# Kernel tuning notes

Hardware: AMD Instinct MI355X
Metric: run time of the kernel (lower is better)

## Reference

```python
import jax, jax.numpy as jnp
import numpy as np
from jax import lax

DN = ('NCHW', 'OIHW', 'NCHW')

def _winit(key, fan_in, shape):
    return (jax.random.uniform(key, shape) - 0.5) * 2 * 2.4 / fan_in ** 0.5

def setup_inputs() -> dict:
    key = jax.random.key(0)
    ks = jax.random.split(key, 6)
    B = 131072
    x = jax.random.normal(ks[0], (B, 1, 16, 16), dtype=jnp.float32)
    H1w = _winit(ks[1], 5 * 5 * 1, (12, 1, 5, 5))
    H1b = jnp.zeros((12, 8, 8), jnp.float32)
    H2w = _winit(ks[2], 5 * 5 * 8, (12, 8, 5, 5))
    H2b = jnp.zeros((12, 4, 4), jnp.float32)
    H3w = _winit(ks[3], 4 * 4 * 12, (4 * 4 * 12, 30))
    H3b = jnp.zeros((30,), jnp.float32)
    outw = _winit(ks[4], 30, (30, 10))
    outb = jnp.zeros((10,), jnp.float32)
    return {"x": x, "H1w": H1w, "H1b": H1b, "H2w": H2w, "H2b": H2b,
            "H3w": H3w, "H3b": H3b, "outw": outw, "outb": outb}

def _pad_m1(x):
    # constant pad of 2 on H and W with value -1.0
    return jnp.pad(x, ((0, 0), (0, 0), (2, 2), (2, 2)), constant_values=-1.0)

def _conv_s2(x, w):
    return lax.conv_general_dilated(x, w, window_strides=(2, 2),
                                    padding='VALID', dimension_numbers=DN)

def reference(x, H1w, H1b, H2w, H2b, H3w, H3b, outw, outb):
    # eval mode: no roll augmentation, dropout is identity
    x = _pad_m1(x)                                   # [B,1,20,20]
    x = _conv_s2(x, H1w) + H1b                       # [B,12,8,8]
    x = jax.nn.relu(x)
    x = _pad_m1(x)                                   # [B,12,12,12]
    s1 = _conv_s2(x[:, 0:8], H2w[0:4])               # [B,4,4,4]
    s2 = _conv_s2(x[:, 4:12], H2w[4:8])              # [B,4,4,4]
    s3 = _conv_s2(jnp.concatenate((x[:, 0:4], x[:, 8:12]), axis=1), H2w[8:12])
    x = jnp.concatenate((s1, s2, s3), axis=1) + H2b  # [B,12,4,4]
    x = jax.nn.relu(x)
    x = x.reshape(x.shape[0], -1)                    # [B,192]
    x = jax.nn.relu(x @ H3w + H3b)                   # [B,30]
    return x @ outw + outb                           # [B,10]
```

## Files before the change

### kernel.cpp

```cpp
#include <hip/hip_runtime.h>
#include <hip/hip_fp16.h>

typedef _Float16 f16x8 __attribute__((ext_vector_type(8)));
typedef float f32x4 __attribute__((ext_vector_type(4)));

union U4H8 { uint4 u; f16x8 h; };
__device__ inline f16x8 asH(uint4 u){ U4H8 x; x.u = u; return x.h; }
__device__ inline unsigned int pk(float a, float b){
    __half2 h = __floats2half2_rn(a, b);
    union { __half2 h; unsigned int u; } c; c.h = h; return c.u;
}
__device__ inline unsigned int pkr(float a, float b){
    return pk(fmaxf(a, 0.f), fmaxf(b, 0.f));
}
__device__ inline unsigned short h16(float a){
    union { __half h; unsigned short s; } c; c.h = __float2half(a); return c.s;
}

#define NFRAG 28
#define WS_B1 7168
#define WS_B2 8192
#define WS_B3 8448
#define WS_B4 8960

__global__ __launch_bounds__(256) void build_tables(
    const float* __restrict__ H1w, const float* __restrict__ H1b,
    const float* __restrict__ H2w, const float* __restrict__ H2b,
    const float* __restrict__ H3w, const float* __restrict__ H3b,
    const float* __restrict__ outw, const float* __restrict__ outb,
    unsigned int* __restrict__ ws)
{
    const int t = threadIdx.x, b = blockIdx.x;
    float* wsf = (float*)ws;

    if (b < NFRAG) {
        if (t < 64) {
            const int lane = t, ch = lane >> 4, oc = lane & 15;
            const int fi = b;
            unsigned short us[8];
            for (int j = 0; j < 8; ++j) {
                float w = 0.f;
                if (fi < 2) {
                    int kh = fi * 4 + ch;
                    if (kh < 5 && j < 5 && oc < 12) w = H1w[oc * 25 + kh * 5 + j];
                } else if (fi < 15) {
                    int kk = fi - 2;
                    int tap = kk * 2 + (ch >> 1);
                    int ic = (ch & 1) * 8 + j;
                    if (tap < 25 && oc < 12) {
                        int kh = tap / 5, kw = tap % 5;
                        int q = oc >> 2, icl = -1;
                        if (q == 0)      { if (ic < 8) icl = ic; }
                        else if (q == 1) { if (ic >= 4 && ic < 12) icl = ic - 4; }
                        else             { if (ic < 4) icl = ic;
                                           else if (ic >= 8 && ic < 12) icl = ic - 4; }
                        if (icl >= 0) w = H2w[((oc * 8 + icl) * 5 + kh) * 5 + kw];
                    }
                } else if (fi < 27) {
                    int idx = fi - 15, nt = idx / 6, kk = idx % 6;
                    int k = kk * 32 + ch * 8 + j;
                    int pos = k / 12, oc2 = k % 12;
                    int col = nt * 16 + oc;
                    if (col < 30) w = H3w[(oc2 * 16 + pos) * 30 + col];
                } else {
                    int k = ch * 8 + j;
                    if (k < 30 && oc < 10) w = outw[k * 10 + oc];
                }
                us[j] = h16(w);
            }
            uint4 u;
            u.x = us[0] | ((unsigned int)us[1] << 16);
            u.y = us[2] | ((unsigned int)us[3] << 16);
            u.z = us[4] | ((unsigned int)us[5] << 16);
            u.w = us[6] | ((unsigned int)us[7] << 16);
            ((uint4*)ws)[fi * 64 + lane] = u;
        }
    } else if (b == NFRAG) {
        for (int idx = t; idx < 1024; idx += 256) {
            int e = idx >> 6, l2 = idx & 63;
            int tt = e >> 2, r = e & 3;
            int oc = 4 * (l2 >> 4) + r, m2 = l2 & 15;
            int oh = 2 * tt + (m2 >> 3), ow = m2 & 7;
            float v = 0.f;
            if (oc < 12) {
                v = H1b[oc * 64 + oh * 8 + ow];
                for (int kh = 0; kh < 5; ++kh)
                    for (int kw = 0; kw < 5; ++kw) {
                        int rr = 2 * oh + kh, cc = 2 * ow + kw;
                        if (rr < 2 || rr >= 18 || cc < 2 || cc >= 18)
                            v -= H1w[oc * 25 + kh * 5 + kw];
                    }
            }
            wsf[WS_B1 + e * 64 + l2] = v;
        }
    } else {
        {
            int e = t >> 6, l2 = t & 63;
            int oc = 4 * (l2 >> 4) + e, m2 = l2 & 15;
            int oh = m2 >> 2, ow = m2 & 3;
            float v = 0.f;
            if (oc < 12) {
                v = H2b[oc * 16 + oh * 4 + ow];
                for (int icl = 0; icl < 8; ++icl)
                    for (int kh = 0; kh < 5; ++kh)
                        for (int kw = 0; kw < 5; ++kw) {
                            int rr = 2 * oh + kh - 2, cc = 2 * ow + kw - 2;
                            if (rr < 0 || rr >= 8 || cc < 0 || cc >= 8)
                                v -= H2w[((oc * 8 + icl) * 5 + kh) * 5 + kw];
                        }
            }
            wsf[WS_B2 + e * 64 + l2] = v;
        }
        for (int i = t; i < 512; i += 256) {
            int e = i >> 6, l2 = i & 63;
            int nt = e >> 2, r = e & 3, ch = l2 >> 4;
            int j = nt * 16 + 4 * ch + r;
            wsf[WS_B3 + e * 64 + l2] = (j < 30) ? H3b[j] : 0.f;
        }
        {
            int e = t >> 6, l2 = t & 63, ch = l2 >> 4;
            int j = 4 * ch + e;
            wsf[WS_B4 + e * 64 + l2] = (j < 10) ? outb[j] : 0.f;
        }
    }
}

#define H2B 36864
#define H3B 39936
__global__ __launch_bounds__(256, 4) void modernnet_mfma(
    const float* __restrict__ x, const unsigned int* __restrict__ ws,
    float* __restrict__ out)
{
    __shared__ uint4 lds4[2528];
    char* L = (char*)lds4;
    const int t = threadIdx.x, wave = t >> 6, l = t & 63;
    const int ch = l >> 4, m = l & 15;
    char* base = L + wave * 9216;
    const int sblk = blockIdx.x * 8;
    const int s0 = sblk + wave * 2;

    const uint4* fr = (const uint4*)ws;
    const float* wsf = (const float*)ws;

    uint4 c1b0 = fr[0 * 64 + l], c1b1 = fr[1 * 64 + l];
    f32x4 b1f[4];
    #pragma unroll
    for (int tt = 0; tt < 4; ++tt)
        #pragma unroll
        for (int r = 0; r < 4; ++r) b1f[tt][r] = wsf[WS_B1 + (tt * 4 + r) * 64 + l];

    {
        uint4 z; z.x = z.y = z.z = z.w = 0u;
        ((uint4*)base)[l] = z;
        if (l < 56) ((uint4*)base)[64 + l] = z;
    }

    {
        const float* xp = x + (size_t)s0 * 256 + l * 8;
        float4 v0 = *(const float4*)xp;
        float4 v1 = *(const float4*)(xp + 4);
        int sI = l >> 5, idx = l & 31;
        int r = idx >> 1, c = (idx & 1) * 8;
        char* dst = base + sI * 960 + (r + 2) * 48 + (c + 2) * 2;
        ((unsigned int*)dst)[0] = pk(v0.x, v0.y);
        ((unsigned int*)dst)[1] = pk(v0.z, v0.w);
        ((unsigned int*)dst)[2] = pk(v1.x, v1.y);
        ((unsigned int*)dst)[3] = pk(v1.z, v1.w);
    }

    uint4 rd[2][5];
    #pragma unroll
    for (int s = 0; s < 2; ++s)
        #pragma unroll
        for (int i = 0; i < 5; ++i) {
            const int cho = (i < 4) ? ch * 48 : 0;
            const unsigned int* p = (const unsigned int*)
                (base + s * 960 + (2 * i + (m >> 3)) * 96 + (m & 7) * 4 + cho);
            rd[s][i] = make_uint4(p[0], p[1], p[2], p[3]);
        }
    f32x4 acc1[8];
    #pragma unroll
    for (int i = 0; i < 8; ++i) {
        const int s = i >> 2, tt = i & 3;
        f32x4 acc = b1f[tt];
        acc = __builtin_amdgcn_mfma_f32_16x16x32_f16(asH(c1b0), asH(rd[s][tt]), acc, 0, 0, 0);
        acc = __builtin_amdgcn_mfma_f32_16x16x32_f16(asH(c1b1), asH(rd[s][tt + 1]), acc, 0, 0, 0);
        acc1[i] = acc;
    }

    #pragma unroll
    for (int i = 0; i < 8; ++i) {
        const int s = i >> 2, tt = i & 3;
        const int pos = (2 * tt + (m >> 3) + 2) * 12 + (m & 7) + 2;
        const int off = ((pos << 5) + ch * 8) ^ ((pos & 12) << 2);
        unsigned int w0 = pkr(acc1[i][0], acc1[i][1]);
        unsigned int w1 = pkr(acc1[i][2], acc1[i][3]);
        *(uint2*)(base + s * 4608 + off) = make_uint2(w0, w1);
    }

    int c2off[13];
    {
        const int mb = 24 * (m >> 2) + 2 * (m & 3);
        const int hb = (ch & 1) << 4;
        const int sel = (ch >> 1) & 1;
        #pragma unroll
        for (int kk = 0; kk < 13; ++kk) {
            const int t0 = 2 * kk;
            const int t1 = (2 * kk + 1 <= 24) ? 2 * kk + 1 : 24;
            const int p0 = (t0 / 5) * 12 + (t0 % 5);
            const int p1 = (t1 / 5) * 12 + (t1 % 5);
            int pos = mb + (sel ? p1 : p0);
            c2off[kk] = ((pos << 5) + hb) ^ ((pos & 12) << 2);
        }
    }

    uint4 c2b[13];
    #pragma unroll
    for (int kk = 0; kk < 13; ++kk) c2b[kk] = fr[(2 + kk) * 64 + l];
    f32x4 b2f;
    #pragma unroll
    for (int r = 0; r < 4; ++r) b2f[r] = wsf[WS_B2 + r * 64 + l];

    {
        uint4 z; z.x = z.y = z.z = z.w = 0u;
        #pragma unroll
        for (int k2 = 0; k2 < 5; ++k2) {
            int idx = l + k2 * 64;
            int smp = (idx >= 160) ? 1 : 0;
            int ci = idx - smp * 160;
            int pi = ci >> 1, half = ci & 1;
            int pos;
            if (pi < 24) pos = pi;
            else if (pi < 48) pos = pi + 96;
            else {
                int q = pi - 48;
                int c = q & 3; c = (c < 2) ? c : c + 8;
                pos = (2 + (q >> 2)) * 12 + c;
            }
            int off = ((pos << 5) + (half << 4)) ^ ((pos & 12) << 2);
            *(uint4*)(base + smp * 4608 + off) = z;
        }
    }

    {
        const char* h0 = base;
        const char* h1 = base + 4608;
        f32x4 a0 = b2f, a1 = b2f;
        #pragma unroll
        for (int kk = 0; kk < 13; ++kk) {
            uint4 r0 = *(const uint4*)(h0 + c2off[kk]);
            uint4 r1 = *(const uint4*)(h1 + c2off[kk]);
            a0 = __builtin_amdgcn_mfma_f32_16x16x32_f16(asH(c2b[kk]), asH(r0), a0, 0, 0, 0);
            a1 = __builtin_amdgcn_mfma_f32_16x16x32_f16(asH(c2b[kk]), asH(r1), a1, 0, 0, 0);
        }
        if (ch < 3) {
            const int sl0 = wave * 2, sl1 = wave * 2 + 1;
            const int off = m * 24 + ch * 8;
            unsigned int w0 = pkr(a0[0], a0[1]);
            unsigned int w1 = pkr(a0[2], a0[3]);
            *(uint2*)(L + H2B + sl0 * 384 + (off ^ (sl0 << 4))) = make_uint2(w0, w1);
            w0 = pkr(a1[0], a1[1]);
            w1 = pkr(a1[2], a1[3]);
            *(uint2*)(L + H2B + sl1 * 384 + (off ^ (sl1 << 4))) = make_uint2(w0, w1);
        }
    }

    uint4 afc[6];
    if (wave < 2) {
        #pragma unroll
        for (int kk = 0; kk < 6; ++kk) afc[kk] = fr[(15 + wave * 6 + kk) * 64 + l];
    }

    __syncthreads();

    if (wave < 2) {
        const int nt = wave;
        const int slot = m & 7;
        f32x4 acc;
        #pragma unroll
        for (int r = 0; r < 4; ++r) acc[r] = wsf[WS_B3 + (nt * 4 + r) * 64 + l];
        #pragma unroll
        for (int kk = 0; kk < 6; ++kk) {
            uint4 bb = *(const uint4*)(L + H2B + slot * 384 +
                                       ((kk * 64 + ch * 16) ^ (slot << 4)));
            acc = __builtin_amdgcn_mfma_f32_16x16x32_f16(asH(afc[kk]), asH(bb), acc, 0, 0, 0);
        }
        if (m < 8) {
            unsigned int w0 = pkr(acc[0], acc[1]);
            unsigned int w1 = pkr(acc[2], acc[3]);
            *(uint2*)(L + H3B + m * 64 + nt * 32 + ch * 8) = make_uint2(w0, w1);
        }
    }

    __syncthreads();

    if (wave == 0) {
        uint4 aw = fr[27 * 64 + l];
        uint4 bb = *(const uint4*)(L + H3B + (m & 7) * 64 + ch * 16);
        f32x4 acc;
        #pragma unroll
        for (int r = 0; r < 4; ++r) acc[r] = wsf[WS_B4 + r * 64 + l];
        acc = __builtin_amdgcn_mfma_f32_16x16x32_f16(asH(aw), asH(bb), acc, 0, 0, 0);
        if (m < 8) {
            float* op = out + (size_t)(sblk + m) * 10 + 4 * ch;
            if (ch < 2) {
                *(float2*)op       = make_float2(acc[0], acc[1]);
                *(float2*)(op + 2) = make_float2(acc[2], acc[3]);
            } else if (ch == 2) {
                *(float2*)op       = make_float2(acc[0], acc[1]);
            }
        }
    }
}

extern "C" void kernel_launch(void* const* d_in, const int* in_sizes, int n_in,
                              void* d_out, int out_size, void* d_ws, size_t ws_size,
                              hipStream_t stream) {
    const float* x    = (const float*)d_in[0];
    const float* H1w  = (const float*)d_in[1];
    const float* H1b  = (const float*)d_in[2];
    const float* H2w  = (const float*)d_in[3];
    const float* H2b  = (const float*)d_in[4];
    const float* H3w  = (const float*)d_in[5];
    const float* H3b  = (const float*)d_in[6];
    const float* outw = (const float*)d_in[7];
    const float* outb = (const float*)d_in[8];
    float* outp = (float*)d_out;
    unsigned int* ws = (unsigned int*)d_ws;

    build_tables<<<30, 256, 0, stream>>>(H1w, H1b, H2w, H2b, H3w, H3b, outw, outb, ws);

    const int B = in_sizes[0] / 256;
    const int blocks = B / 8;
    modernnet_mfma<<<blocks, 256, 0, stream>>>(x, ws, outp);
}
```

Measured before the change: 89.66 us.

## Pack conv1 activations densely in LDS and hoist global loads earlier

```diff
diff --git a/kernel.cpp b/kernel.cpp
--- a/kernel.cpp
+++ b/kernel.cpp
@@ -125,23 +125,28 @@
     }
 }
 
-#define H2B 36864
-#define H3B 39936
+#define REG   3456
+#define H2B   27648
+#define H3B   30720
 __global__ __launch_bounds__(256, 4) void modernnet_mfma(
     const float* __restrict__ x, const unsigned int* __restrict__ ws,
     float* __restrict__ out)
 {
-    __shared__ uint4 lds4[2528];
+    __shared__ uint4 lds4[1952];
     char* L = (char*)lds4;
     const int t = threadIdx.x, wave = t >> 6, l = t & 63;
     const int ch = l >> 4, m = l & 15;
-    char* base = L + wave * 9216;
+    char* base = L + wave * (2 * REG);
     const int sblk = blockIdx.x * 8;
     const int s0 = sblk + wave * 2;
 
     const uint4* fr = (const uint4*)ws;
     const float* wsf = (const float*)ws;
 
+    const float* xp = x + (size_t)s0 * 256 + l * 8;
+    float4 xv0 = *(const float4*)xp;
+    float4 xv1 = *(const float4*)(xp + 4);
+
     uint4 c1b0 = fr[0 * 64 + l], c1b1 = fr[1 * 64 + l];
     f32x4 b1f[4];
     #pragma unroll
@@ -149,23 +154,54 @@
         #pragma unroll
         for (int r = 0; r < 4; ++r) b1f[tt][r] = wsf[WS_B1 + (tt * 4 + r) * 64 + l];
 
+    int c2off[13];
+    {
+        const int mb = 24 * (m >> 2) + 2 * (m & 3);
+        const int hb = (ch & 1) << 4;
+        const int sel = (ch >> 1) & 1;
+        #pragma unroll
+        for (int kk = 0; kk < 13; ++kk) {
+            const int t0 = 2 * kk;
+            const int t1 = (2 * kk + 1 <= 24) ? 2 * kk + 1 : 24;
+            const int p0 = (t0 / 5) * 12 + (t0 % 5);
+            const int p1 = (t1 / 5) * 12 + (t1 % 5);
+            int pos = mb + (sel ? p1 : p0);
+            c2off[kk] = pos * 24 + hb;
+        }
+    }
+
+    uint4 c2b[13];
+    #pragma unroll
+    for (int kk = 0; kk < 13; ++kk) c2b[kk] = fr[(2 + kk) * 64 + l];
+    f32x4 b2f;
+    #pragma unroll
+    for (int r = 0; r < 4; ++r) b2f[r] = wsf[WS_B2 + r * 64 + l];
+
     {
         uint4 z; z.x = z.y = z.z = z.w = 0u;
-        ((uint4*)base)[l] = z;
-        if (l < 56) ((uint4*)base)[64 + l] = z;
-    }
-
-    {
-        const float* xp = x + (size_t)s0 * 256 + l * 8;
-        float4 v0 = *(const float4*)xp;
-        float4 v1 = *(const float4*)(xp + 4);
+        if (l < 60) {
+            ((uint4*)base)[l] = z;
+            *(uint4*)(base + REG + l * 16) = z;
+        }
+    }
+
+    {
         int sI = l >> 5, idx = l & 31;
         int r = idx >> 1, c = (idx & 1) * 8;
-        char* dst = base + sI * 960 + (r + 2) * 48 + (c + 2) * 2;
+        const float4 va = sI ? xv1 : xv0;
+        const float4 vb = sI ? *(const float4*)(xp + 4) : xv0;
+        (void)vb;
+        char* dst = base + sI * REG + (r + 2) * 48 + (c + 2) * 2;
+        const float4 v0 = sI ? xv1 : xv0;
+        (void)va;
         ((unsigned int*)dst)[0] = pk(v0.x, v0.y);
         ((unsigned int*)dst)[1] = pk(v0.z, v0.w);
-        ((unsigned int*)dst)[2] = pk(v1.x, v1.y);
-        ((unsigned int*)dst)[3] = pk(v1.z, v1.w);
+        float4 v1 = sI ? *(const float4*)(xp + 4) : *(const float4*)(xp + 4);
+        (void)v1;
+        ((unsigned int*)dst)[2] = pk(xv1.x, xv1.y);
+        ((unsigned int*)dst)[3] = pk(xv1.z, xv1.w);
+        ((unsigned int*)dst)[0] = pk(xv0.x, xv0.y);
+        ((unsigned int*)dst)[1] = pk(xv0.z, xv0.w);
     }
 
     uint4 rd[2][5];
@@ -175,7 +211,7 @@
         for (int i = 0; i < 5; ++i) {
             const int cho = (i < 4) ? ch * 48 : 0;
             const unsigned int* p = (const unsigned int*)
-                (base + s * 960 + (2 * i + (m >> 3)) * 96 + (m & 7) * 4 + cho);
+                (base + s * REG + (2 * i + (m >> 3)) * 96 + (m & 7) * 4 + cho);
             rd[s][i] = make_uint4(p[0], p[1], p[2], p[3]);
         }
     f32x4 acc1[8];
@@ -191,65 +227,47 @@
     #pragma unroll
     for (int i = 0; i < 8; ++i) {
         const int s = i >> 2, tt = i & 3;
-        const int pos = (2 * tt + (m >> 3) + 2) * 12 + (m & 7) + 2;
-        const int off = ((pos << 5) + ch * 8) ^ ((pos & 12) << 2);
-        unsigned int w0 = pkr(acc1[i][0], acc1[i][1]);
-        unsigned int w1 = pkr(acc1[i][2], acc1[i][3]);
-        *(uint2*)(base + s * 4608 + off) = make_uint2(w0, w1);
-    }
-
-    int c2off[13];
-    {
-        const int mb = 24 * (m >> 2) + 2 * (m & 3);
-        const int hb = (ch & 1) << 4;
-        const int sel = (ch >> 1) & 1;
+        if (ch < 3) {
+            const int pos = (2 * tt + (m >> 3) + 2) * 12 + (m & 7) + 2;
+            unsigned int w0 = pkr(acc1[i][0], acc1[i][1]);
+            unsigned int w1 = pkr(acc1[i][2], acc1[i][3]);
+            *(uint2*)(base + s * REG + pos * 24 + ch * 8) = make_uint2(w0, w1);
+        }
+    }
+
+    {
+        uint4 z; z.x = z.y = z.z = z.w = 0u;
+        #pragma unroll
+        for (int k2 = 0; k2 < 4; ++k2) {
+            int idx = l + k2 * 64;
+            if (idx < 240) {
+                int smp = (idx >= 120) ? 1 : 0;
+                int i1 = idx - smp * 120;
+                int off;
+                if (i1 < 36)      off = i1 * 16;
+                else if (i1 < 72) off = 2880 + (i1 - 36) * 16;
+                else {
+                    int q = i1 - 72;
+                    int row = 2 + q / 6, c6 = q % 6;
+                    off = row * 288 + (c6 < 3 ? c6 * 16 : 192 + c6 * 16);
+                }
+                *(uint4*)(base + smp * REG + off) = z;
+            }
+        }
+    }
+
+    {
+        const char* h0 = base;
+        const char* h1 = base + REG;
+        f32x4 a0 = b2f, a1 = b2f;
         #pragma unroll
         for (int kk = 0; kk < 13; ++kk) {
-            const int t0 = 2 * kk;
-            const int t1 = (2 * kk + 1 <= 24) ? 2 * kk + 1 : 24;
-            const int p0 = (t0 / 5) * 12 + (t0 % 5);
-            const int p1 = (t1 / 5) * 12 + (t1 % 5);
-            int pos = mb + (sel ? p1 : p0);
-            c2off[kk] = ((pos << 5) + hb) ^ ((pos & 12) << 2);
-        }
-    }
-
-    uint4 c2b[13];
-    #pragma unroll
-    for (int kk = 0; kk < 13; ++kk) c2b[kk] = fr[(2 + kk) * 64 + l];
-    f32x4 b2f;
-    #pragma unroll
-    for (int r = 0; r < 4; ++r) b2f[r] = wsf[WS_B2 + r * 64 + l];
-
-    {
-        uint4 z; z.x = z.y = z.z = z.w = 0u;
-        #pragma unroll
-        for (int k2 = 0; k2 < 5; ++k2) {
-            int idx = l + k2 * 64;
-            int smp = (idx >= 160) ? 1 : 0;
-            int ci = idx - smp * 160;
-            int pi = ci >> 1, half = ci & 1;
-            int pos;
-            if (pi < 24) pos = pi;
-            else if (pi < 48) pos = pi + 96;
-            else {
-                int q = pi - 48;
-                int c = q & 3; c = (c < 2) ? c : c + 8;
-                pos = (2 + (q >> 2)) * 12 + c;
-            }
-            int off = ((pos << 5) + (half << 4)) ^ ((pos & 12) << 2);
-            *(uint4*)(base + smp * 4608 + off) = z;
-        }
-    }
-
-    {
-        const char* h0 = base;
-        const char* h1 = base + 4608;
-        f32x4 a0 = b2f, a1 = b2f;
-        #pragma unroll
-        for (int kk = 0; kk < 13; ++kk) {
-            uint4 r0 = *(const uint4*)(h0 + c2off[kk]);
-            uint4 r1 = *(const uint4*)(h1 + c2off[kk]);
+            uint2 r0a = *(const uint2*)(h0 + c2off[kk]);
+            uint2 r0b = *(const uint2*)(h0 + c2off[kk] + 8);
+            uint2 r1a = *(const uint2*)(h1 + c2off[kk]);
+            uint2 r1b = *(const uint2*)(h1 + c2off[kk] + 8);
+            uint4 r0 = make_uint4(r0a.x, r0a.y, r0b.x, r0b.y);
+            uint4 r1 = make_uint4(r1a.x, r1a.y, r1b.x, r1b.y);
             a0 = __builtin_amdgcn_mfma_f32_16x16x32_f16(asH(c2b[kk]), asH(r0), a0, 0, 0, 0);
             a1 = __builtin_amdgcn_mfma_f32_16x16x32_f16(asH(c2b[kk]), asH(r1), a1, 0, 0, 0);
         }
```

Result: slower. 98.49 us (+9.9%).
